# Performance work log

Hardware: AMD Instinct MI355X
Metric: run time of the kernel (lower is better)

The kernel has to match this reference:

```python
import jax, jax.numpy as jnp
import numpy as np


def setup_inputs() -> dict:
    key = jax.random.key(0)
    k1, k2 = jax.random.split(key)
    x = jax.random.normal(k1, (32, 128, 112, 112), dtype=jnp.float32)
    weight = jax.random.normal(k2, (256, 128, 3, 3), dtype=jnp.float32)
    return {"x": x, "weight": weight}


def reference(x, weight):
    # Equivalent to torch unfold + einsum: valid (no padding), stride-1
    # cross-correlation conv2d with no bias.
    # x: [B, Cin, H, W], weight: [Cout, Cin, kh, kw] -> [B, Cout, H-kh+1, W-kw+1]
    return jax.lax.conv_general_dilated(
        x, weight,
        window_strides=(1, 1),
        padding="VALID",
        dimension_numbers=("NCHW", "OIHW", "NCHW"),
    )
```

## Files before the change

kernel.cpp:

```cpp
#include <hip/hip_runtime.h>

typedef __attribute__((ext_vector_type(8))) short short8;
typedef __attribute__((ext_vector_type(4))) float f32x4;
typedef unsigned int u32;

#define CIN   128
#define COUT  256
#define H     112
#define W     112
#define OH    110
#define OW    110
#define KHW   9
#define TH    8
#define TW    32
#define IHH   10
#define IWW   34
#define NPIX  340
#define XB    (NPIX*8*16)
#define WB    16384

__device__ __forceinline__ short f2b(float f) {
  unsigned u = __builtin_bit_cast(unsigned, f);
  unsigned r = (u + 0x7FFFu + ((u >> 16) & 1u)) >> 16;
  return (short)r;
}

__device__ __forceinline__ void gload16(const void* g, void* l) {
  __builtin_amdgcn_global_load_lds(
      (const __attribute__((address_space(1))) u32*)g,
      (__attribute__((address_space(3))) u32*)l, 16, 0, 0);
}


template<bool XT, bool WT>
__global__ __launch_bounds__(256, 2)
void conv_main(const float* __restrict__ x, const float* __restrict__ wgt,
               const short* __restrict__ wt, const short* __restrict__ xt,
               const short* __restrict__ zp, float* __restrict__ out) {
  __shared__ __align__(16) char smem[XB + 2*WB];
  char* sx = smem;
  char* sw = smem + XB;

  const int tid = threadIdx.x;

  const int nb  = gridDim.x;
  const int swz = (blockIdx.x & 7) * (nb >> 3) + (blockIdx.x >> 3);
  const int b    = swz / 112;
  const int rem  = swz - b * 112;
  const int cblk = rem / 56;
  const int rem2 = rem - cblk * 56;
  const int t_w  = rem2 / 14;
  const int t_h  = rem2 - t_w * 14;
  const int h0 = t_h * TH, w0 = t_w * TW;

  auto stage_x = [&](int hh) {
    if (XT) {
      const short* xtb = xt + (size_t)b * (H*W*CIN);
      #pragma unroll
      for (int it = 0; it < 11; ++it) {
        int u = it*256 + tid;
        if (u < 8*NPIX) {
          int p = u >> 3;
          int Geff = (u & 7) ^ (p & 7);
          int iy = p / IWW, ix = p - iy * IWW;
          int gy = h0 + iy, gx = w0 + ix;
          const short* src = (gy < H && gx < W)
              ? xtb + ((size_t)gy*W + gx)*CIN + hh*64 + Geff*8
              : zp;
          gload16(src, sx + u*16);
        }
      }
    } else {
      const float* xh = x + (size_t)b * CIN * (H*W) + (size_t)(hh*64) * (H*W);
      for (int u = tid; u < 8 * NPIX; u += 256) {
        int G = u / NPIX, p = u - G * NPIX;
        int iy = p / IWW, ix = p - iy * IWW;
        int gy = h0 + iy, gx = w0 + ix;
        short8 v = {0,0,0,0,0,0,0,0};
        if (gy < H && gx < W) {
          const float* s = xh + (size_t)(G*8) * (H*W) + gy * W + gx;
          #pragma unroll
          for (int j = 0; j < 8; ++j) v[j] = f2b(s[j * (H*W)]);
        }
        *(short8*)(sx + p*128 + ((G ^ (p & 7)) << 4)) = v;
      }
    }
  };

  auto stage_w = [&](int st, int buf) {
    int hh = st / 9, tap = st - hh * 9;
    if (WT) {
      const short* base = wt + (size_t)tap * (COUT*CIN)
                             + (size_t)(cblk*128) * CIN + hh * 64;
      #pragma unroll
      for (int it = 0; it < 4; ++it) {
        int slot = it * 256 + tid;
        int c = slot >> 3, gsw = (slot & 7) ^ (c & 7);
        gload16(base + c * CIN + gsw * 8, sw + buf*WB + slot * 16);
      }
    } else {
      #pragma unroll
      for (int it = 0; it < 4; ++it) {
        int slot = it * 256 + tid;
        int c = slot >> 3, gsw = (slot & 7) ^ (c & 7);
        int cout = cblk*128 + c;
        short8 v;
        #pragma unroll
        for (int j = 0; j < 8; ++j) {
          int cin = hh*64 + gsw*8 + j;
          v[j] = f2b(wgt[cout*(CIN*KHW) + cin*KHW + tap]);
        }
        *(short8*)(sw + buf*WB + slot * 16) = v;
      }
    }
  };

  const int lane = tid & 63;
  const int wid  = tid >> 6;
  const int wm = wid >> 1;
  const int wn = wid & 1;
  const int l15 = lane & 15;
  const int kgrp = lane >> 4;

  f32x4 acc[4][8] = {};

  stage_x(0);
  stage_w(0, 0);
  __syncthreads();

  for (int st = 0; st < 18; ++st) {
    if (st + 1 < 18) stage_w(st + 1, (st + 1) & 1);

    const int tap = st % 9;
    const int kh = tap / 3, kw = tap - (tap/3)*3;
    const char* swb = sw + (st & 1) * WB;

    #pragma unroll
    for (int s = 0; s < 2; ++s) {
      const int g = s*4 + kgrp;
      const int aslot = (g ^ (l15 & 7)) << 4;
      short8 a[4];
      #pragma unroll
      for (int mi = 0; mi < 4; ++mi)
        a[mi] = *(const short8*)(swb + (wm*64 + mi*16 + l15) * 128 + aslot);
      short8 bf[8];
      #pragma unroll
      for (int ni = 0; ni < 8; ++ni) {
        int p = (4*wn + (ni >> 1) + kh) * IWW + (ni & 1)*16 + l15 + kw;
        bf[ni] = *(const short8*)(sx + p*128 + ((g ^ (p & 7)) << 4));
      }
      #pragma unroll
      for (int mi = 0; mi < 4; ++mi)
        #pragma unroll
        for (int ni = 0; ni < 8; ++ni)
          acc[mi][ni] = __builtin_amdgcn_mfma_f32_16x16x32_bf16(a[mi], bf[ni], acc[mi][ni], 0, 0, 0);
    }

    if (st == 8) {
      __syncthreads();
      stage_x(1);
      __syncthreads();
    } else {
      __syncthreads();
    }
  }

  float* ob = out + (size_t)b * COUT * (OH*OW);
  #pragma unroll
  for (int ni = 0; ni < 8; ++ni) {
    int oh = h0 + 4*wn + (ni >> 1);
    int ow = w0 + (ni & 1)*16 + l15;
    if (oh < OH && ow < OW) {
      #pragma unroll
      for (int mi = 0; mi < 4; ++mi) {
        #pragma unroll
        for (int r = 0; r < 4; ++r) {
          int cout = cblk*128 + wm*64 + mi*16 + kgrp*4 + r;
          ob[(size_t)cout*(OH*OW) + oh*OW + ow] = acc[mi][ni][r];
        }
      }
    }
  }
}

__global__ void wprep(const float* __restrict__ wgt, short* __restrict__ wt,
                      short* __restrict__ zp) {
  int idx = blockIdx.x * 256 + threadIdx.x;
  if (idx < 128) zp[idx] = 0;
  if (idx >= KHW*COUT*CIN) return;
  int khw  = idx / (COUT*CIN);
  int rem  = idx - khw*(COUT*CIN);
  int cout = rem >> 7, cin = rem & 127;
  wt[idx] = f2b(wgt[cout*(CIN*KHW) + cin*KHW + khw]);
}

__global__ __launch_bounds__(256)
void xprep(const float* __restrict__ x, short* __restrict__ xt) {
  __shared__ short lsh[CIN * 113];
  const int bh = blockIdx.x;
  const int b = bh / H, h = bh - b * H;
  const float* src = x + ((size_t)b * CIN * H + h) * W;
  for (int u = threadIdx.x; u < CIN * W; u += 256) {
    int c = u / W, w = u - c * W;
    lsh[c * 113 + w] = f2b(src[(size_t)c * (H*W) + w]);
  }
  __syncthreads();
  short* dst = xt + (size_t)bh * (W * CIN);
  for (int o = threadIdx.x; o < W * CIN / 8; o += 256) {
    int w = o >> 4, s = o & 15;
    short8 v;
    #pragma unroll
    for (int j = 0; j < 8; ++j) v[j] = lsh[(s*8 + j) * 113 + w];
    *(short8*)(dst + o * 8) = v;
  }
}

extern "C" void kernel_launch(void* const* d_in, const int* in_sizes, int n_in,
                              void* d_out, int out_size, void* d_ws, size_t ws_size,
                              hipStream_t stream) {
  const float* x   = (const float*)d_in[0];
  const float* wgt = (const float*)d_in[1];
  float* out = (float*)d_out;
  const size_t wt_bytes = (size_t)(KHW*COUT*CIN) * sizeof(short);
  const size_t zp_bytes = 256;
  const size_t xt_bytes = (size_t)32 * H * W * CIN * sizeof(short);
  dim3 grid(3584);
  if (ws_size >= wt_bytes + zp_bytes + xt_bytes) {
    short* wt = (short*)d_ws;
    short* zp = (short*)((char*)d_ws + wt_bytes);
    short* xt = (short*)((char*)d_ws + wt_bytes + zp_bytes);
    wprep<<<(KHW*COUT*CIN + 255)/256, 256, 0, stream>>>(wgt, wt, zp);
    xprep<<<32 * H, 256, 0, stream>>>(x, xt);
    conv_main<true, true><<<grid, 256, 0, stream>>>(x, wgt, wt, xt, zp, out);
  } else if (ws_size >= wt_bytes + zp_bytes) {
    short* wt = (short*)d_ws;
    short* zp = (short*)((char*)d_ws + wt_bytes);
    wprep<<<(KHW*COUT*CIN + 255)/256, 256, 0, stream>>>(wgt, wt, zp);
    conv_main<false, true><<<grid, 256, 0, stream>>>(x, wgt, wt, nullptr, zp, out);
  } else {
    conv_main<false, false><<<grid, 256, 0, stream>>>(x, wgt, nullptr, nullptr, nullptr, out);
  }
}
```

Measured before the change: 348.1 us.

## Reorder conv loop by kw to reuse input fragments across kh taps

The tap loop is restructured so that, for each channel half and each kw, a 6x2 window of input fragments is loaded from LDS into registers once and reused across the three kh taps. This roughly halves the LDS reads for the input operand. The weight pipeline is split into 36 stages instead of 18, and MFMA issue is wrapped in s_setprio. The trade-off is that each stage still stages the full 64-channel weight slice but uses only half of it, which doubles weight global traffic and the number of barriers. Holding the window also raises register pressure.

```diff
diff --git a/kernel.cpp b/kernel.cpp
--- a/kernel.cpp
+++ b/kernel.cpp
@@ -87,8 +87,7 @@
     }
   };
 
-  auto stage_w = [&](int st, int buf) {
-    int hh = st / 9, tap = st - hh * 9;
+  auto stage_w = [&](int tap, int hh, int buf) {
     if (WT) {
       const short* base = wt + (size_t)tap * (COUT*CIN)
                              + (size_t)(cblk*128) * CIN + hh * 64;
@@ -125,42 +124,57 @@
   f32x4 acc[4][8] = {};
 
   stage_x(0);
-  stage_w(0, 0);
+  stage_w(0, 0, 0);
   __syncthreads();
 
-  for (int st = 0; st < 18; ++st) {
-    if (st + 1 < 18) stage_w(st + 1, (st + 1) & 1);
-
-    const int tap = st % 9;
-    const int kh = tap / 3, kw = tap - (tap/3)*3;
-    const char* swb = sw + (st & 1) * WB;
-
-    #pragma unroll
+  int stg = 0;
+  for (int hh = 0; hh < 2; ++hh) {
     for (int s = 0; s < 2; ++s) {
-      const int g = s*4 + kgrp;
-      const int aslot = (g ^ (l15 & 7)) << 4;
-      short8 a[4];
-      #pragma unroll
-      for (int mi = 0; mi < 4; ++mi)
-        a[mi] = *(const short8*)(swb + (wm*64 + mi*16 + l15) * 128 + aslot);
-      short8 bf[8];
-      #pragma unroll
-      for (int ni = 0; ni < 8; ++ni) {
-        int p = (4*wn + (ni >> 1) + kh) * IWW + (ni & 1)*16 + l15 + kw;
-        bf[ni] = *(const short8*)(sx + p*128 + ((g ^ (p & 7)) << 4));
-      }
-      #pragma unroll
-      for (int mi = 0; mi < 4; ++mi)
-        #pragma unroll
-        for (int ni = 0; ni < 8; ++ni)
-          acc[mi][ni] = __builtin_amdgcn_mfma_f32_16x16x32_bf16(a[mi], bf[ni], acc[mi][ni], 0, 0, 0);
-    }
-
-    if (st == 8) {
-      __syncthreads();
+      const int g0 = s * 4 + kgrp;
+      const int aslot = (g0 ^ (l15 & 7)) << 4;
+      #pragma unroll
+      for (int kw = 0; kw < 3; ++kw) {
+        short8 win[6][2];
+        #pragma unroll
+        for (int ri = 0; ri < 6; ++ri) {
+          #pragma unroll
+          for (int cg = 0; cg < 2; ++cg) {
+            int p = (4*wn + ri) * IWW + cg*16 + l15 + kw;
+            win[ri][cg] = *(const short8*)(sx + p*128 + ((g0 ^ (p & 7)) << 4));
+          }
+        }
+        #pragma unroll
+        for (int kh = 0; kh < 3; ++kh) {
+          {
+            int ns = stg + 1;
+            if (ns < 36) {
+              int nhh = ns / 18, nr = ns % 9;
+              int ntap = (nr % 3) * 3 + (nr / 3);
+              stage_w(ntap, nhh, ns & 1);
+            }
+          }
+          const char* swb = sw + (stg & 1) * WB;
+          short8 a[4];
+          #pragma unroll
+          for (int mi = 0; mi < 4; ++mi)
+            a[mi] = *(const short8*)(swb + (wm*64 + mi*16 + l15) * 128 + aslot);
+
+          __builtin_amdgcn_s_setprio(1);
+          #pragma unroll
+          for (int mi = 0; mi < 4; ++mi)
+            #pragma unroll
+            for (int ni = 0; ni < 8; ++ni)
+              acc[mi][ni] = __builtin_amdgcn_mfma_f32_16x16x32_bf16(
+                  a[mi], win[(ni >> 1) + kh][ni & 1], acc[mi][ni], 0, 0, 0);
+          __builtin_amdgcn_s_setprio(0);
+
+          __syncthreads();
+          ++stg;
+        }
+      }
+    }
+    if (hh == 0) {
       stage_x(1);
-      __syncthreads();
-    } else {
       __syncthreads();
     }
   }
```

Measured after the change: 678.7 us. +95.0%, slower.
